# Optimization experiments

Hardware: AMD Instinct MI355X
Metric: run time of the kernel (lower is better)

Reference implementation:

```python
import jax, jax.numpy as jnp
import numpy as np

B, S, D = 4, 8192, 512


def setup_inputs() -> dict:
    key = jax.random.key(0)
    k1, k2, k3 = jax.random.split(key, 3)
    input_real = jax.random.normal(k1, (B, S, D), dtype=jnp.float32)
    input_imag = jax.random.normal(k2, (B, S, D), dtype=jnp.float32)
    weight = jax.random.uniform(k3, (B, S), dtype=jnp.float32)
    return {"input_real": input_real, "input_imag": input_imag, "weight": weight}


def reference(input_real, input_imag, weight):
    # Original: sum_s w[b,s] * (r_s r_s^T + i_s i_s^T)  and  sum_s w[b,s] * (i_s r_s^T - r_s i_s^T).
    # Algebraically equal to weighted Gram GEMMs X^T diag(w) Y; avoids the [B,S,D,D] intermediate.
    def wgram(x, y):
        # [B,S,D] x [B,S] x [B,S,D] -> [B,D,D]
        return jnp.einsum('bsd,bs,bse->bde', x, weight, y)

    output_r = wgram(input_real, input_real) + wgram(input_imag, input_imag)
    output_i = wgram(input_imag, input_real) - wgram(input_real, input_imag)
    return (output_r, output_i)
```

## Files before the change

kernel.cpp:

```cpp
#include <hip/hip_runtime.h>
#include <cstdint>
#include <cstddef>

#define NB 4
#define NS 8192
#define ND 512
#define NP 1024
#define BK 32

typedef __bf16 bf16x8 __attribute__((ext_vector_type(8)));
typedef float f32x4 __attribute__((ext_vector_type(4)));

union FragU { uint4 u; bf16x8 h; };

__device__ __forceinline__ unsigned short bf16rne(float x) {
  unsigned int u = __builtin_bit_cast(unsigned int, x);
  u += 0x7FFFu + ((u >> 16) & 1u);
  return (unsigned short)(u >> 16);
}

__device__ __forceinline__ void gload16(const void* g, void* l) {
  __builtin_amdgcn_global_load_lds(
      (const __attribute__((address_space(1))) unsigned int*)g,
      (__attribute__((address_space(3))) unsigned int*)l, 16, 0, 0);
}

__global__ __launch_bounds__(256)
void k_prep(const float* __restrict__ R, const float* __restrict__ I,
            const float* __restrict__ W, unsigned short* __restrict__ Yt) {
  __shared__ unsigned short L[64][66];
  const int t   = threadIdx.x;
  const int blk = blockIdx.x;
  const int sb  = blk & 127;
  const int pb  = (blk >> 7) & 15;
  const int b   = blk >> 11;
  const float* src = (pb < 8) ? R : I;
  const int col0 = (pb & 7) * 64;
  const int s0 = sb * 64;
  const int dl = (t & 15) * 4;
  const int sl0 = t >> 4;
#pragma unroll
  for (int r = 0; r < 4; ++r) {
    const int sl = sl0 + r * 16;
    const int s  = s0 + sl;
    const float sw = sqrtf(W[b * NS + s]);
    const float4 v = *(const float4*)(src + (size_t)(b * NS + s) * ND + col0 + dl);
    L[sl][dl + 0] = bf16rne(v.x * sw);
    L[sl][dl + 1] = bf16rne(v.y * sw);
    L[sl][dl + 2] = bf16rne(v.z * sw);
    L[sl][dl + 3] = bf16rne(v.w * sw);
  }
  __syncthreads();
  const int pl0 = t >> 3;
  const int sc  = (t & 7) * 8;
#pragma unroll
  for (int r = 0; r < 2; ++r) {
    const int pl = pl0 + r * 32;
    uint4 o;
    o.x = (unsigned)L[sc + 0][pl] | ((unsigned)L[sc + 1][pl] << 16);
    o.y = (unsigned)L[sc + 2][pl] | ((unsigned)L[sc + 3][pl] << 16);
    o.z = (unsigned)L[sc + 4][pl] | ((unsigned)L[sc + 5][pl] << 16);
    o.w = (unsigned)L[sc + 6][pl] | ((unsigned)L[sc + 7][pl] << 16);
    const int pg = pb * 64 + pl;
    *(uint4*)(Yt + (size_t)(b * NP + pg) * NS + (s0 + sc)) = o;
  }
}

__global__ __launch_bounds__(256, 2)
void k_gemm(const unsigned short* __restrict__ Yt, float* __restrict__ part,
            float* __restrict__ outp, int ksteps, int direct) {
  __shared__ uint4 lds4[2048];
  char* lds = (char*)lds4;
  const int bid   = blockIdx.x;
  const int pos   = bid & 15;
  const int b     = (bid >> 4) & 3;
  const int split = bid >> 6;
  const int tm = pos >> 2, tn = pos & 3;
  const int t = threadIdx.x;
  const int l = t & 63;
  const int w = t >> 6;

  const int cj = l & 7;
  const int jj = l >> 3;
  const int ec = cj ^ jj;
  const int rbase = w * 16 + 2 * jj + (ec >> 2);
  const int colo  = (ec & 3) * 8;

  const int prow[4] = { tm * 128, 512 + tm * 128, tn * 128, 512 + tn * 128 };
  const unsigned short* gsrc[8];
#pragma unroll
  for (int tI = 0; tI < 4; ++tI)
#pragma unroll
    for (int i = 0; i < 2; ++i)
      gsrc[tI * 2 + i] = Yt + (size_t)(b * NP + prow[tI] + i * 64 + rbase) * NS
                         + (size_t)split * ((size_t)ksteps * BK) + colo;

  const int g  = l >> 4;
  const int e_ = l & 1;
  const int q  = (l >> 1) & 7;
  const int ibase = ((l & 15) >> 1) * 128 + ((64 * e_ + 16 * g) ^ (q << 4));

  const int wm = w & 1, wn = w >> 1;
  const int mfb = wm * 4096;
  const int nfb = wn * 4096;

  f32x4 accr[4][4], acci[4][4];
  const f32x4 zz = {0.f, 0.f, 0.f, 0.f};
#pragma unroll
  for (int a = 0; a < 4; ++a)
#pragma unroll
    for (int c = 0; c < 4; ++c) { accr[a][c] = zz; acci[a][c] = zz; }

  for (int ks = 0; ks < ksteps; ++ks) {
#pragma unroll
    for (int u = 0; u < 8; ++u) {
      const int tI = u >> 1, ii = u & 1;
      gload16(gsrc[u], lds + tI * 8192 + ii * 4096 + w * 1024);
      gsrc[u] += BK;
    }
    __syncthreads();
    FragU ar[4], ai[4];
#pragma unroll
    for (int mf = 0; mf < 4; ++mf) {
      ar[mf].u = *(const uint4*)(lds +         mfb + mf * 1024 + ibase);
      ai[mf].u = *(const uint4*)(lds + 8192  + mfb + mf * 1024 + ibase);
    }
#pragma unroll
    for (int nf = 0; nf < 4; ++nf) {
      FragU br, bi, bin;
      br.u = *(const uint4*)(lds + 16384 + nfb + nf * 1024 + ibase);
      bi.u = *(const uint4*)(lds + 24576 + nfb + nf * 1024 + ibase);
      bin.u.x = bi.u.x ^ 0x80008000u;
      bin.u.y = bi.u.y ^ 0x80008000u;
      bin.u.z = bi.u.z ^ 0x80008000u;
      bin.u.w = bi.u.w ^ 0x80008000u;
#pragma unroll
      for (int mf = 0; mf < 4; ++mf) {
        accr[mf][nf] = __builtin_amdgcn_mfma_f32_16x16x32_bf16(ar[mf].h, br.h,  accr[mf][nf], 0, 0, 0);
        accr[mf][nf] = __builtin_amdgcn_mfma_f32_16x16x32_bf16(ai[mf].h, bi.h,  accr[mf][nf], 0, 0, 0);
        acci[mf][nf] = __builtin_amdgcn_mfma_f32_16x16x32_bf16(ai[mf].h, br.h,  acci[mf][nf], 0, 0, 0);
        acci[mf][nf] = __builtin_amdgcn_mfma_f32_16x16x32_bf16(ar[mf].h, bin.h, acci[mf][nf], 0, 0, 0);
      }
    }
    __syncthreads();
  }

  const int lr = (l >> 4) * 4;
  const int lc = l & 15;
  if (direct) {
    const size_t ob = (size_t)b * 262144;
#pragma unroll
    for (int mf = 0; mf < 4; ++mf)
#pragma unroll
      for (int nf = 0; nf < 4; ++nf)
#pragma unroll
        for (int r = 0; r < 4; ++r) {
          const int row = tm * 128 + wm * 64 + mf * 16 + lr + r;
          const int col = tn * 128 + wn * 64 + nf * 16 + lc;
          outp[          ob + (size_t)row * 512 + col] = accr[mf][nf][r];
          outp[1048576 + ob + (size_t)row * 512 + col] = acci[mf][nf][r];
        }
  } else {
    const size_t baser = ((size_t)(split * 2 + 0) * 4 + b) * (16 * 16384)
                         + (size_t)pos * 16384;
    const size_t basei = baser + (size_t)4 * 16 * 16384;
#pragma unroll
    for (int mf = 0; mf < 4; ++mf)
#pragma unroll
      for (int nf = 0; nf < 4; ++nf)
#pragma unroll
        for (int r = 0; r < 4; ++r) {
          const int mi = wm * 64 + mf * 16 + lr + r;
          const int ni = wn * 64 + nf * 16 + lc;
          part[baser + (size_t)mi * 128 + ni] = accr[mf][nf][r];
          part[basei + (size_t)mi * 128 + ni] = acci[mf][nf][r];
        }
  }
}

__global__ __launch_bounds__(256)
void k_reduce(const float* __restrict__ part, float* __restrict__ out, int nsplit) {
  const int tid = blockIdx.x * 256 + threadIdx.x;
  float a = 0.f;
  for (int s = 0; s < nsplit; ++s)
    a += part[(size_t)s * 2097152 + tid];
  const int o    = tid >> 20;
  const int rem  = tid & 1048575;
  const int b    = rem >> 18;
  const int rem2 = rem & 262143;
  const int pos  = rem2 >> 14;
  const int e    = rem2 & 16383;
  const int tm = pos >> 2, tn = pos & 3;
  const int mi = e >> 7, ni = e & 127;
  out[(size_t)o * 1048576 + (size_t)b * 262144
      + (size_t)(tm * 128 + mi) * 512 + (tn * 128 + ni)] = a;
}

__global__ __launch_bounds__(256)
void k_fallback(const float* __restrict__ R, const float* __restrict__ I,
                const float* __restrict__ W, float* __restrict__ out) {
  __shared__ float Rd[64][32], Id[64][32], Re[64][32], Ie[64][32];
  const int blk = blockIdx.x;
  const int et = blk & 15, dt = (blk >> 4) & 15, b = blk >> 8;
  const int d0 = dt * 32, e0 = et * 32;
  const int t = threadIdx.x;
  const int dd = t >> 3;
  const int ee0 = (t & 7) * 4;
  float ar[4] = {0,0,0,0}, ai[4] = {0,0,0,0};
  for (int s0 = 0; s0 < NS; s0 += 64) {
#pragma unroll
    for (int k = 0; k < 8; ++k) {
      const int idx = t + k * 256;
      const int row = idx >> 5, col = idx & 31;
      const float sw = sqrtf(W[b * NS + s0 + row]);
      const size_t gr = (size_t)(b * NS + s0 + row) * ND;
      Rd[row][col] = R[gr + d0 + col] * sw;
      Id[row][col] = I[gr + d0 + col] * sw;
      Re[row][col] = R[gr + e0 + col] * sw;
      Ie[row][col] = I[gr + e0 + col] * sw;
    }
    __syncthreads();
    for (int s = 0; s < 64; ++s) {
      const float rd = Rd[s][dd], id = Id[s][dd];
#pragma unroll
      for (int j = 0; j < 4; ++j) {
        const float re = Re[s][ee0 + j], ie = Ie[s][ee0 + j];
        ar[j] += rd * re + id * ie;
        ai[j] += id * re - rd * ie;
      }
    }
    __syncthreads();
  }
  const size_t ob = (size_t)b * 262144;
#pragma unroll
  for (int j = 0; j < 4; ++j) {
    out[          ob + (size_t)(d0 + dd) * 512 + e0 + ee0 + j] = ar[j];
    out[1048576 + ob + (size_t)(d0 + dd) * 512 + e0 + ee0 + j] = ai[j];
  }
}

extern "C" void kernel_launch(void* const* d_in, const int* in_sizes, int n_in,
                              void* d_out, int out_size, void* d_ws, size_t ws_size,
                              hipStream_t stream) {
  const float* R = (const float*)d_in[0];
  const float* I = (const float*)d_in[1];
  const float* W = (const float*)d_in[2];
  float* out = (float*)d_out;
  const size_t ytBytes  = (size_t)NB * NP * NS * 2;
  const size_t perSplit = (size_t)2 * NB * 16 * 16384 * 4;

  if (ws_size < ytBytes) {
    k_fallback<<<dim3(NB * 16 * 16), dim3(256), 0, stream>>>(R, I, W, out);
    return;
  }

  unsigned short* Yt = (unsigned short*)d_ws;
  float* part = (float*)((char*)d_ws + ytBytes);
  int SPLIT = 8;
  while (SPLIT > 1 && ytBytes + (size_t)SPLIT * perSplit > ws_size) SPLIT >>= 1;

  k_prep<<<dim3(NB * 16 * 128), dim3(256), 0, stream>>>(R, I, W, Yt);
  if (SPLIT > 1) {
    k_gemm<<<dim3(64 * SPLIT), dim3(256), 0, stream>>>(Yt, part, nullptr,
                                                       256 / SPLIT, 0);
    k_reduce<<<dim3(8192), dim3(256), 0, stream>>>(part, out, SPLIT);
  } else {
    k_gemm<<<dim3(64), dim3(256), 0, stream>>>(Yt, nullptr, out, 256, 1);
  }
}
```

Measured before the change: 265.9 us.

## Exploit Hermitian symmetry: compute lower-triangle tiles, double-buffer LDS, mirror outputs

Both outputs have a fixed symmetry: the real part is symmetric and the imaginary part is antisymmetric. The GEMM therefore computes only the 10 lower-triangular 128x128 tile pairs per batch instead of all 16. A new mirror kernel fills the upper tiles by transposing and, for the imaginary part, negating. The GEMM main loop also gains LDS double buffering, prefetching the next K-slice while MFMAs run on the current one, and the default split-K rises from 8 to 16. The trade-offs are an extra launch, an extra output read/write pass, doubled LDS use that may lower occupancy, and removal of the no-split direct path.

Result: faster. 246.8 us (-7.2%).

```diff
diff --git a/kernel.cpp b/kernel.cpp
--- a/kernel.cpp
+++ b/kernel.cpp
@@ -68,14 +68,17 @@
 
 __global__ __launch_bounds__(256, 2)
 void k_gemm(const unsigned short* __restrict__ Yt, float* __restrict__ part,
-            float* __restrict__ outp, int ksteps, int direct) {
-  __shared__ uint4 lds4[2048];
+            int ksteps) {
+  __shared__ uint4 lds4[4096];
   char* lds = (char*)lds4;
+  static const int TMp[10] = {0,1,1,2,2,2,3,3,3,3};
+  static const int TNp[10] = {0,0,1,0,1,2,0,1,2,3};
   const int bid   = blockIdx.x;
-  const int pos   = bid & 15;
-  const int b     = (bid >> 4) & 3;
-  const int split = bid >> 6;
-  const int tm = pos >> 2, tn = pos & 3;
+  const int pos40 = bid % 40;
+  const int split = bid / 40;
+  const int b     = pos40 / 10;
+  const int p     = pos40 % 10;
+  const int tm = TMp[p], tn = TNp[p];
   const int t = threadIdx.x;
   const int l = t & 63;
   const int w = t >> 6;
@@ -88,12 +91,15 @@
 
   const int prow[4] = { tm * 128, 512 + tm * 128, tn * 128, 512 + tn * 128 };
   const unsigned short* gsrc[8];
+  int dstoff[8];
 #pragma unroll
   for (int tI = 0; tI < 4; ++tI)
 #pragma unroll
-    for (int i = 0; i < 2; ++i)
+    for (int i = 0; i < 2; ++i) {
       gsrc[tI * 2 + i] = Yt + (size_t)(b * NP + prow[tI] + i * 64 + rbase) * NS
                          + (size_t)split * ((size_t)ksteps * BK) + colo;
+      dstoff[tI * 2 + i] = tI * 8192 + i * 4096 + w * 1024;
+    }
 
   const int g  = l >> 4;
   const int e_ = l & 1;
@@ -111,25 +117,29 @@
 #pragma unroll
     for (int c = 0; c < 4; ++c) { accr[a][c] = zz; acci[a][c] = zz; }
 
+#pragma unroll
+  for (int u = 0; u < 8; ++u) { gload16(gsrc[u], lds + dstoff[u]); gsrc[u] += BK; }
+  __syncthreads();
+
+  int cur = 0;
   for (int ks = 0; ks < ksteps; ++ks) {
-#pragma unroll
-    for (int u = 0; u < 8; ++u) {
-      const int tI = u >> 1, ii = u & 1;
-      gload16(gsrc[u], lds + tI * 8192 + ii * 4096 + w * 1024);
-      gsrc[u] += BK;
-    }
-    __syncthreads();
+    const int cbase = cur * 32768;
+    const int nbase = cbase ^ 32768;
+    if (ks + 1 < ksteps) {
+#pragma unroll
+      for (int u = 0; u < 8; ++u) { gload16(gsrc[u], lds + nbase + dstoff[u]); gsrc[u] += BK; }
+    }
     FragU ar[4], ai[4];
 #pragma unroll
     for (int mf = 0; mf < 4; ++mf) {
-      ar[mf].u = *(const uint4*)(lds +         mfb + mf * 1024 + ibase);
-      ai[mf].u = *(const uint4*)(lds + 8192  + mfb + mf * 1024 + ibase);
+      ar[mf].u = *(const uint4*)(lds + cbase +        mfb + mf * 1024 + ibase);
+      ai[mf].u = *(const uint4*)(lds + cbase + 8192 + mfb + mf * 1024 + ibase);
     }
 #pragma unroll
     for (int nf = 0; nf < 4; ++nf) {
       FragU br, bi, bin;
-      br.u = *(const uint4*)(lds + 16384 + nfb + nf * 1024 + ibase);
-      bi.u = *(const uint4*)(lds + 24576 + nfb + nf * 1024 + ibase);
+      br.u = *(const uint4*)(lds + cbase + 16384 + nfb + nf * 1024 + ibase);
+      bi.u = *(const uint4*)(lds + cbase + 24576 + nfb + nf * 1024 + ibase);
       bin.u.x = bi.u.x ^ 0x80008000u;
       bin.u.y = bi.u.y ^ 0x80008000u;
       bin.u.z = bi.u.z ^ 0x80008000u;
@@ -143,57 +153,79 @@
       }
     }
     __syncthreads();
-  }
-
+    cur ^= 1;
+  }
+
+  const size_t baser = ((size_t)(split * 40 + pos40) * 2 + 0) * 16384;
+  const size_t basei = baser + 16384;
   const int lr = (l >> 4) * 4;
   const int lc = l & 15;
-  if (direct) {
-    const size_t ob = (size_t)b * 262144;
-#pragma unroll
-    for (int mf = 0; mf < 4; ++mf)
-#pragma unroll
-      for (int nf = 0; nf < 4; ++nf)
-#pragma unroll
-        for (int r = 0; r < 4; ++r) {
-          const int row = tm * 128 + wm * 64 + mf * 16 + lr + r;
-          const int col = tn * 128 + wn * 64 + nf * 16 + lc;
-          outp[          ob + (size_t)row * 512 + col] = accr[mf][nf][r];
-          outp[1048576 + ob + (size_t)row * 512 + col] = acci[mf][nf][r];
-        }
-  } else {
-    const size_t baser = ((size_t)(split * 2 + 0) * 4 + b) * (16 * 16384)
-                         + (size_t)pos * 16384;
-    const size_t basei = baser + (size_t)4 * 16 * 16384;
-#pragma unroll
-    for (int mf = 0; mf < 4; ++mf)
-#pragma unroll
-      for (int nf = 0; nf < 4; ++nf)
-#pragma unroll
-        for (int r = 0; r < 4; ++r) {
-          const int mi = wm * 64 + mf * 16 + lr + r;
-          const int ni = wn * 64 + nf * 16 + lc;
-          part[baser + (size_t)mi * 128 + ni] = accr[mf][nf][r];
-          part[basei + (size_t)mi * 128 + ni] = acci[mf][nf][r];
-        }
-  }
+#pragma unroll
+  for (int mf = 0; mf < 4; ++mf)
+#pragma unroll
+    for (int nf = 0; nf < 4; ++nf)
+#pragma unroll
+      for (int r = 0; r < 4; ++r) {
+        const int mi = wm * 64 + mf * 16 + lr + r;
+        const int ni = wn * 64 + nf * 16 + lc;
+        part[baser + (size_t)mi * 128 + ni] = accr[mf][nf][r];
+        part[basei + (size_t)mi * 128 + ni] = acci[mf][nf][r];
+      }
 }
 
 __global__ __launch_bounds__(256)
 void k_reduce(const float* __restrict__ part, float* __restrict__ out, int nsplit) {
-  const int tid = blockIdx.x * 256 + threadIdx.x;
+  static const int TMp[10] = {0,1,1,2,2,2,3,3,3,3};
+  static const int TNp[10] = {0,0,1,0,1,2,0,1,2,3};
+  const int idx = blockIdx.x * 256 + threadIdx.x;
+  const int ni = idx & 127;
+  const int mi = (idx >> 7) & 127;
+  const int o  = (idx >> 14) & 1;
+  const int bp = idx >> 15;
+  const int b = bp / 10, p = bp % 10;
+  const size_t stride = (size_t)40 * 2 * 16384;
+  size_t base = ((size_t)bp * 2 + o) * 16384 + (size_t)mi * 128 + ni;
   float a = 0.f;
   for (int s = 0; s < nsplit; ++s)
-    a += part[(size_t)s * 2097152 + tid];
-  const int o    = tid >> 20;
-  const int rem  = tid & 1048575;
-  const int b    = rem >> 18;
-  const int rem2 = rem & 262143;
-  const int pos  = rem2 >> 14;
-  const int e    = rem2 & 16383;
-  const int tm = pos >> 2, tn = pos & 3;
-  const int mi = e >> 7, ni = e & 127;
-  out[(size_t)o * 1048576 + (size_t)b * 262144
-      + (size_t)(tm * 128 + mi) * 512 + (tn * 128 + ni)] = a;
+    a += part[base + (size_t)s * stride];
+  const int d = TMp[p] * 128 + mi;
+  const int e = TNp[p] * 128 + ni;
+  out[(size_t)o * 1048576 + (size_t)b * 262144 + (size_t)d * 512 + e] = a;
+}
+
+__global__ __launch_bounds__(256)
+void k_mirror(float* __restrict__ out) {
+  __shared__ float T[64][65];
+  static const int UM[6] = {0,0,0,1,1,2};
+  static const int UN[6] = {1,2,3,2,3,3};
+  const int m = blockIdx.x;
+  const int sub = m & 3;
+  const int b   = (m >> 2) & 3;
+  const int o   = (m >> 4) & 1;
+  const int u   = m >> 5;
+  const int d0 = UM[u] * 128 + (sub & 1) * 64;
+  const int e0 = UN[u] * 128 + ((sub >> 1) & 1) * 64;
+  const float sign = o ? -1.f : 1.f;
+  float* base = out + (size_t)o * 1048576 + (size_t)b * 262144;
+  const int t  = threadIdx.x;
+  const int c4 = (t & 15) * 4;
+  const int r0 = t >> 4;
+#pragma unroll
+  for (int i = 0; i < 4; ++i) {
+    const int r = r0 + i * 16;
+    const float4 v = *(const float4*)(base + (size_t)(e0 + r) * 512 + d0 + c4);
+    T[c4 + 0][r] = v.x; T[c4 + 1][r] = v.y;
+    T[c4 + 2][r] = v.z; T[c4 + 3][r] = v.w;
+  }
+  __syncthreads();
+#pragma unroll
+  for (int i = 0; i < 4; ++i) {
+    const int r = r0 + i * 16;
+    float4 wv;
+    wv.x = sign * T[r][c4 + 0]; wv.y = sign * T[r][c4 + 1];
+    wv.z = sign * T[r][c4 + 2]; wv.w = sign * T[r][c4 + 3];
+    *(float4*)(base + (size_t)(d0 + r) * 512 + e0 + c4) = wv;
+  }
 }
 
 __global__ __launch_bounds__(256)
@@ -247,24 +279,20 @@
   const float* W = (const float*)d_in[2];
   float* out = (float*)d_out;
   const size_t ytBytes  = (size_t)NB * NP * NS * 2;
-  const size_t perSplit = (size_t)2 * NB * 16 * 16384 * 4;
-
-  if (ws_size < ytBytes) {
+  const size_t perSplit = (size_t)40 * 2 * 16384 * 4;
+
+  int SPLIT = 16;
+  while (SPLIT > 2 && ytBytes + (size_t)SPLIT * perSplit > ws_size) SPLIT >>= 1;
+  if (ytBytes + (size_t)SPLIT * perSplit > ws_size) {
     k_fallback<<<dim3(NB * 16 * 16), dim3(256), 0, stream>>>(R, I, W, out);
     return;
   }
 
   unsigned short* Yt = (unsigned short*)d_ws;
   float* part = (float*)((char*)d_ws + ytBytes);
-  int SPLIT = 8;
-  while (SPLIT > 1 && ytBytes + (size_t)SPLIT * perSplit > ws_size) SPLIT >>= 1;
 
   k_prep<<<dim3(NB * 16 * 128), dim3(256), 0, stream>>>(R, I, W, Yt);
-  if (SPLIT > 1) {
-    k_gemm<<<dim3(64 * SPLIT), dim3(256), 0, stream>>>(Yt, part, nullptr,
-                                                       256 / SPLIT, 0);
-    k_reduce<<<dim3(8192), dim3(256), 0, stream>>>(part, out, SPLIT);
-  } else {
-    k_gemm<<<dim3(64), dim3(256), 0, stream>>>(Yt, nullptr, out, 256, 1);
-  }
-}
+  k_gemm<<<dim3(40 * SPLIT), dim3(256), 0, stream>>>(Yt, part, 256 / SPLIT);
+  k_reduce<<<dim3(5120), dim3(256), 0, stream>>>(part, out, SPLIT);
+  k_mirror<<<dim3(192), dim3(256), 0, stream>>>(out);
+}
```
